# Performance work log

Measured on AMD Instinct MI355X. Metric: run time of the kernel, lower is better.

Reference implementation:

```python
import jax, jax.numpy as jnp
import numpy as np

N_NODES = 2048
N_EDGES = 16384
D_FEAT = 4  # 2*D_FEAT = 8 qubit angles per edge

# TTN circuit gate sequence: ('ry', wire, theta_idx) or ('cx', control, target)
OPS = [("ry",1,0),("ry",2,1),("cx",1,2),
       ("ry",5,2),("ry",6,3),("cx",6,5),
       ("ry",0,4),("ry",1,5),("cx",0,1),
       ("ry",2,6),("ry",3,7),("cx",3,2),
       ("ry",4,8),("ry",5,9),("cx",4,5),
       ("ry",6,10),("ry",7,11),("cx",7,6),
       ("ry",2,12),("ry",5,13),("cx",2,5),
       ("ry",1,14),("ry",2,15),("cx",1,2),
       ("ry",5,16),("ry",6,17),("cx",6,5),
       ("ry",2,18),("ry",5,19),("cx",2,5),
       ("ry",5,20)]

def setup_inputs() -> dict:
    key = jax.random.key(0)
    k1, k2, k3, k4 = jax.random.split(key, 4)
    X = jax.random.normal(k1, (N_NODES, D_FEAT), dtype=jnp.float32)
    Ri = jax.random.normal(k2, (N_NODES, N_EDGES), dtype=jnp.float32)
    Ro = jax.random.normal(k3, (N_NODES, N_EDGES), dtype=jnp.float32)
    theta = jax.random.uniform(k4, (21,), dtype=jnp.float32) * (4.0 * np.pi)
    return {"X": X, "Ri": Ri, "Ro": Ro, "theta": theta}

def _ry(state, w, th):
    # state: [B, 2,2,2,2,2,2,2,2]; apply RY(th) on wire w (real rotation)
    c = jnp.cos(0.5 * th)
    s = jnp.sin(0.5 * th)
    a0 = jnp.take(state, 0, axis=w + 1)
    a1 = jnp.take(state, 1, axis=w + 1)
    return jnp.stack([c * a0 - s * a1, s * a0 + c * a1], axis=w + 1)

def _cnot(state, c, t):
    s0 = jnp.take(state, 0, axis=c + 1)  # control=0 branch: unchanged
    s1 = jnp.take(state, 1, axis=c + 1)  # control=1 branch: flip target
    t_ax = t + 1 if t < c else t  # axis shift after removing control axis
    s1 = jnp.flip(s1, axis=t_ax)
    return jnp.stack([s0, s1], axis=c + 1)

def _circuit(angles, theta):
    # angles: [B, 8] per-edge RY encoding angles; all gates real -> real statevector
    B = angles.shape[0]
    half = 0.5 * angles
    amps = jnp.stack([jnp.cos(half), jnp.sin(half)], axis=-1)  # [B, 8, 2], RY(a)|0>
    state = amps[:, 0, :]  # [B, 2]
    for q in range(1, 8):  # product state build-up -> [B, 2^8]
        state = state[..., None] * amps[:, q, :].reshape((B,) + (1,) * q + (2,))
    for op in OPS:
        if op[0] == "ry":
            state = _ry(state, op[1], theta[op[2]])
        else:
            state = _cnot(state, op[1], op[2])
    p = state * state  # probabilities (real amplitudes)
    m = jnp.sum(p, axis=(1, 2, 3, 4, 5, 7, 8))  # marginal over wire 5 -> [B, 2]
    ez = m[:, 0] - m[:, 1]  # <Z_5>
    return (1.0 - ez) / 2.0

def reference(X, Ri, Ro, theta):
    bo = jnp.einsum('ne,nd->ed', Ro, X)  # [E, 4]
    bi = jnp.einsum('ne,nd->ed', Ri, X)  # [E, 4]
    angles = jnp.concatenate([bo, bi], axis=1)  # [E, 8]
    return _circuit(angles, theta)
```

## Files before the change

kernel.cpp:

```cpp
#include <hip/hip_runtime.h>
#include <cstdint>

constexpr int N_NODES  = 2048;
constexpr int N_EDGES  = 16384;
constexpr int NS       = 16;
constexpr int CHUNK    = N_NODES / NS;
constexpr int KSUB     = 4;
constexpr int SUBCHUNK = CHUNK / KSUB;
constexpr int TG       = 64;
constexpr int EPT      = 4;
constexpr int K1_BLOCK = TG * KSUB;
constexpr int GROUPS   = N_EDGES / EPT;

__global__ __launch_bounds__(K1_BLOCK) void k1_partial(
    const float* __restrict__ X,
    const float* __restrict__ Ri,
    const float* __restrict__ Ro,
    float* __restrict__ part)
{
    __shared__ float4 xs[CHUNK];
    __shared__ float  red[KSUB][TG][33];

    const int ns  = blockIdx.y;
    const int n0  = ns * CHUNK;
    const int tid = threadIdx.x;
    const int gl  = tid & (TG - 1);
    const int ks  = tid >> 6;

    if (tid < CHUNK) xs[tid] = reinterpret_cast<const float4*>(X)[n0 + tid];
    __syncthreads();

    const int g = blockIdx.x * TG + gl;
    const float4* Ro4 = reinterpret_cast<const float4*>(Ro);
    const float4* Ri4 = reinterpret_cast<const float4*>(Ri);

    float acc_o[EPT][4];
    float acc_i[EPT][4];
    #pragma unroll
    for (int el = 0; el < EPT; ++el)
        #pragma unroll
        for (int q = 0; q < 4; ++q) { acc_o[el][q] = 0.f; acc_i[el][q] = 0.f; }

    const int kbase = n0 + ks * SUBCHUNK;
    #pragma unroll 8
    for (int k = 0; k < SUBCHUNK; ++k) {
        const int n = kbase + k;
        const float4 ro = Ro4[n * (N_EDGES / 4) + g];
        const float4 ri = Ri4[n * (N_EDGES / 4) + g];
        const float4 x  = xs[n - n0];
        const float roa[EPT] = {ro.x, ro.y, ro.z, ro.w};
        const float ria[EPT] = {ri.x, ri.y, ri.z, ri.w};
        const float xa[4]    = {x.x,  x.y,  x.z,  x.w};
        #pragma unroll
        for (int el = 0; el < EPT; ++el)
            #pragma unroll
            for (int q = 0; q < 4; ++q) {
                acc_o[el][q] = fmaf(roa[el], xa[q], acc_o[el][q]);
                acc_i[el][q] = fmaf(ria[el], xa[q], acc_i[el][q]);
            }
    }

    #pragma unroll
    for (int q = 0; q < 4; ++q)
        #pragma unroll
        for (int el = 0; el < EPT; ++el) {
            red[ks][gl][q * 4 + el]      = acc_o[el][q];
            red[ks][gl][16 + q * 4 + el] = acc_i[el][q];
        }
    __syncthreads();

    if (ks == 0) {
        float sum[32];
        #pragma unroll
        for (int v = 0; v < 32; ++v)
            sum[v] = ((red[0][gl][v] + red[1][gl][v]) +
                      (red[2][gl][v] + red[3][gl][v]));
        #pragma unroll
        for (int el = 0; el < EPT; ++el) {
            const int e = 4 * g + el;
            float4* dst = reinterpret_cast<float4*>(part + ((size_t)ns * N_EDGES + e) * 8);
            dst[0] = make_float4(sum[0 * 4 + el], sum[1 * 4 + el], sum[2 * 4 + el], sum[3 * 4 + el]);
            dst[1] = make_float4(sum[16 + 0 * 4 + el], sum[16 + 1 * 4 + el],
                                 sum[16 + 2 * 4 + el], sum[16 + 3 * 4 + el]);
        }
    }
}

template<int LVL>
__device__ __forceinline__ void build64(float* st, float c, float s) {
    #pragma unroll
    for (int i = (1 << LVL) - 1; i >= 0; --i) {
        const float v = st[i];
        st[2 * i]     = v * c;
        st[2 * i + 1] = v * s;
    }
}

template<int W>
__device__ __forceinline__ void ry64(float* st, float c, float s) {
    constexpr int STRIDE = 1 << (7 - W);
    #pragma unroll
    for (int base = 0; base < 64; base += 2 * STRIDE)
        #pragma unroll
        for (int j = 0; j < STRIDE; ++j) {
            const int i0 = base + j, i1 = i0 + STRIDE;
            const float a0 = st[i0], a1 = st[i1];
            st[i0] = fmaf(c, a0, -(s * a1));
            st[i1] = fmaf(s, a0,   c * a1);
        }
}

__device__ __forceinline__ void ry_cross(float* st, float c, float s, int mask, int mybit) {
    const float ss = mybit ? s : -s;
    #pragma unroll
    for (int j = 0; j < 64; ++j) {
        const float other = __shfl_xor(st[j], mask, 64);
        st[j] = fmaf(c, st[j], ss * other);
    }
}

template<int CB, int TB>
__device__ __forceinline__ void cx_reg(float* st) {
    #pragma unroll
    for (int i = 0; i < 64; ++i)
        if ((i & CB) && !(i & TB)) {
            const float t = st[i]; st[i] = st[i | TB]; st[i | TB] = t;
        }
}

__global__ __launch_bounds__(256, 2) void k2_circuit(
    const float* __restrict__ part,
    const float* __restrict__ theta,
    float* __restrict__ out)
{
    const int tid = threadIdx.x;
    const int sub = tid & 3;
    const int e   = blockIdx.x * 64 + (tid >> 2);
    const int p0  = (sub >> 1) & 1;
    const int p1  = sub & 1;

    float a[8] = {0.f, 0.f, 0.f, 0.f, 0.f, 0.f, 0.f, 0.f};
    #pragma unroll
    for (int r = 0; r < 4; ++r) {
        const int ns = sub * 4 + r;
        const float4* p4 = reinterpret_cast<const float4*>(
            part + ((size_t)ns * N_EDGES + e) * 8);
        const float4 lo = p4[0], hi = p4[1];
        a[0] += lo.x; a[1] += lo.y; a[2] += lo.z; a[3] += lo.w;
        a[4] += hi.x; a[5] += hi.y; a[6] += hi.z; a[7] += hi.w;
    }
    #pragma unroll
    for (int q = 0; q < 8; ++q) {
        a[q] += __shfl_xor(a[q], 1, 64);
        a[q] += __shfl_xor(a[q], 2, 64);
    }

    float st[64];
    {
        float c, s, f;
        sincosf(0.5f * a[0], &s, &c); f  = p0 ? s : c;
        sincosf(0.5f * a[1], &s, &c); f *= p1 ? s : c;
        st[0] = f;
        sincosf(0.5f * a[2], &s, &c); build64<0>(st, c, s);
        sincosf(0.5f * a[3], &s, &c); build64<1>(st, c, s);
        sincosf(0.5f * a[4], &s, &c); build64<2>(st, c, s);
        sincosf(0.5f * a[5], &s, &c); build64<3>(st, c, s);
        sincosf(0.5f * a[6], &s, &c); build64<4>(st, c, s);
        sincosf(0.5f * a[7], &s, &c); build64<5>(st, c, s);
    }

#define THC(IDX) float c_, s_; __sincosf(0.5f * theta[IDX], &s_, &c_)
#define RYL(W, IDX) { THC(IDX); ry64<W>(st, c_, s_); }
#define RY0(IDX)    { THC(IDX); ry_cross(st, c_, s_, 2, p0); }
#define RY1(IDX)    { THC(IDX); ry_cross(st, c_, s_, 1, p1); }

    RY1(0) RYL(2, 1)
    {
        #pragma unroll
        for (int j = 0; j < 32; ++j) {
            const float t0 = st[j], t1 = st[j + 32];
            st[j]      = p1 ? t1 : t0;
            st[j + 32] = p1 ? t0 : t1;
        }
    }
    RYL(5, 2) RYL(6, 3) cx_reg<2, 4>(st);
    RY0(4) RY1(5)
    {
        #pragma unroll
        for (int j = 0; j < 64; ++j) {
            const float other = __shfl_xor(st[j], 1, 64);
            st[j] = p0 ? other : st[j];
        }
    }
    RYL(2, 6) RYL(3, 7) cx_reg<16, 32>(st);
    RYL(4, 8) RYL(5, 9) cx_reg<8, 4>(st);
    RYL(6, 10) RYL(7, 11) cx_reg<1, 2>(st);
    RYL(2, 12) RYL(5, 13) cx_reg<32, 4>(st);
    RY1(14) RYL(2, 15)
    {
        #pragma unroll
        for (int j = 0; j < 32; ++j) {
            const float t0 = st[j], t1 = st[j + 32];
            st[j]      = p1 ? t1 : t0;
            st[j + 32] = p1 ? t0 : t1;
        }
    }
    RYL(5, 16) RYL(6, 17) cx_reg<2, 4>(st);
    RYL(2, 18) RYL(5, 19) cx_reg<32, 4>(st);
    RYL(5, 20)
#undef RYL
#undef RY0
#undef RY1
#undef THC

    float m0 = 0.f, m1 = 0.f;
    #pragma unroll
    for (int j = 0; j < 64; ++j) {
        if (j & 4) m1 = fmaf(st[j], st[j], m1);
        else       m0 = fmaf(st[j], st[j], m0);
    }
    float d = m1 - m0;
    d += __shfl_xor(d, 1, 64);
    d += __shfl_xor(d, 2, 64);
    if (sub == 0) out[e] = 0.5f * (1.0f + d);
}

extern "C" void kernel_launch(void* const* d_in, const int* in_sizes, int n_in,
                              void* d_out, int out_size, void* d_ws, size_t ws_size,
                              hipStream_t stream)
{
    const float* X     = (const float*)d_in[0];
    const float* Ri    = (const float*)d_in[1];
    const float* Ro    = (const float*)d_in[2];
    const float* theta = (const float*)d_in[3];
    float* part = (float*)d_ws;
    float* outp = (float*)d_out;

    dim3 g1(GROUPS / TG, NS);
    k1_partial<<<g1, dim3(K1_BLOCK), 0, stream>>>(X, Ri, Ro, part);
    k2_circuit<<<dim3(N_EDGES / 64), dim3(256), 0, stream>>>(part, theta, outp);
}
```

Before: 60.98 us.

## Replace LDS cross-subchunk reduction with intra-wave shuffles in partial GEMV kernel

Remaps threads so each wave covers 16 edge groups across 4 node sub-ranges, letting the k-split partial sums be reduced with wave shuffles instead of a shared-memory array and block barrier. This drops the large LDS reduction buffer, enabling higher occupancy (launch bounds raised to 4 blocks). The trade-off is shorter contiguous global load segments per wave (256B instead of 1KB) and more shuffle instructions.

```diff
diff --git a/kernel.cpp b/kernel.cpp
--- a/kernel.cpp
+++ b/kernel.cpp
@@ -9,28 +9,28 @@
 constexpr int SUBCHUNK = CHUNK / KSUB;
 constexpr int TG       = 64;
 constexpr int EPT      = 4;
-constexpr int K1_BLOCK = TG * KSUB;
+constexpr int K1_BLOCK = 256;
 constexpr int GROUPS   = N_EDGES / EPT;
 
-__global__ __launch_bounds__(K1_BLOCK) void k1_partial(
+__global__ __launch_bounds__(K1_BLOCK, 4) void k1_partial(
     const float* __restrict__ X,
     const float* __restrict__ Ri,
     const float* __restrict__ Ro,
     float* __restrict__ part)
 {
     __shared__ float4 xs[CHUNK];
-    __shared__ float  red[KSUB][TG][33];
-
     const int ns  = blockIdx.y;
     const int n0  = ns * CHUNK;
     const int tid = threadIdx.x;
-    const int gl  = tid & (TG - 1);
-    const int ks  = tid >> 6;
-
     if (tid < CHUNK) xs[tid] = reinterpret_cast<const float4*>(X)[n0 + tid];
     __syncthreads();
 
-    const int g = blockIdx.x * TG + gl;
+    const int lane = tid & 63;
+    const int wv   = tid >> 6;
+    const int gl   = lane & 15;
+    const int ks   = lane >> 4;
+    const int g    = blockIdx.x * TG + wv * 16 + gl;
+
     const float4* Ro4 = reinterpret_cast<const float4*>(Ro);
     const float4* Ri4 = reinterpret_cast<const float4*>(Ri);
 
@@ -41,13 +41,14 @@
         #pragma unroll
         for (int q = 0; q < 4; ++q) { acc_o[el][q] = 0.f; acc_i[el][q] = 0.f; }
 
-    const int kbase = n0 + ks * SUBCHUNK;
+    const int kbase = ks * SUBCHUNK;
     #pragma unroll 8
     for (int k = 0; k < SUBCHUNK; ++k) {
-        const int n = kbase + k;
-        const float4 ro = Ro4[n * (N_EDGES / 4) + g];
-        const float4 ri = Ri4[n * (N_EDGES / 4) + g];
-        const float4 x  = xs[n - n0];
+        const int kk = kbase + k;
+        const int n  = n0 + kk;
+        const float4 ro = Ro4[(size_t)n * (N_EDGES / 4) + g];
+        const float4 ri = Ri4[(size_t)n * (N_EDGES / 4) + g];
+        const float4 x  = xs[kk];
         const float roa[EPT] = {ro.x, ro.y, ro.z, ro.w};
         const float ria[EPT] = {ri.x, ri.y, ri.z, ri.w};
         const float xa[4]    = {x.x,  x.y,  x.z,  x.w};
@@ -60,28 +61,27 @@
             }
     }
 
+    float sum[32];
     #pragma unroll
     for (int q = 0; q < 4; ++q)
         #pragma unroll
         for (int el = 0; el < EPT; ++el) {
-            red[ks][gl][q * 4 + el]      = acc_o[el][q];
-            red[ks][gl][16 + q * 4 + el] = acc_i[el][q];
-        }
-    __syncthreads();
+            sum[q * 4 + el]      = acc_o[el][q];
+            sum[16 + q * 4 + el] = acc_i[el][q];
+        }
+    #pragma unroll
+    for (int v = 0; v < 32; ++v) {
+        sum[v] += __shfl_xor(sum[v], 16, 64);
+        sum[v] += __shfl_xor(sum[v], 32, 64);
+    }
 
     if (ks == 0) {
-        float sum[32];
-        #pragma unroll
-        for (int v = 0; v < 32; ++v)
-            sum[v] = ((red[0][gl][v] + red[1][gl][v]) +
-                      (red[2][gl][v] + red[3][gl][v]));
         #pragma unroll
         for (int el = 0; el < EPT; ++el) {
             const int e = 4 * g + el;
             float4* dst = reinterpret_cast<float4*>(part + ((size_t)ns * N_EDGES + e) * 8);
-            dst[0] = make_float4(sum[0 * 4 + el], sum[1 * 4 + el], sum[2 * 4 + el], sum[3 * 4 + el]);
-            dst[1] = make_float4(sum[16 + 0 * 4 + el], sum[16 + 1 * 4 + el],
-                                 sum[16 + 2 * 4 + el], sum[16 + 3 * 4 + el]);
+            dst[0] = make_float4(sum[0 + el], sum[4 + el], sum[8 + el], sum[12 + el]);
+            dst[1] = make_float4(sum[16 + el], sum[20 + el], sum[24 + el], sum[28 + el]);
         }
     }
 }
```

After: 61.69 us. About the same (+1.2%).
